# Kernel optimization log

Hardware: AMD Instinct MI355X
Metric: run time of the kernel (lower is better)

The kernel has to match this reference:

```python
import jax, jax.numpy as jnp
import numpy as np

B, S, D_IN = 16, 4096, 1024
H, HD = 8, 64            # num_heads, head_dim
V = H * HD               # value_dim = 512
F_OUT = 120              # forecast_horizon
EPS = 1e-5


def _rotate(x):
    # theta_shift in the source ignores sin/cos: stack((-x2, x1)) and flatten
    x1 = x[..., 0::2]
    x2 = x[..., 1::2]
    return jnp.stack((-x2, x1), axis=-1).reshape(x.shape)


def setup_inputs() -> dict:
    key = jax.random.key(0)
    kx, kq, kk, kv, ko, _ = jax.random.split(key, 6)
    return {
        "x": jax.random.normal(kx, (B, S, D_IN), dtype=jnp.float32),
        "Wq": jax.random.normal(kq, (V, D_IN), dtype=jnp.float32) * 0.02,
        "Wk": jax.random.normal(kk, (V, D_IN), dtype=jnp.float32) * 0.02,
        "Wv": jax.random.normal(kv, (V, D_IN), dtype=jnp.float32) * 0.02,
        "Wout": jax.random.normal(ko, (F_OUT, V), dtype=jnp.float32) * 0.02,
        "gamma": jnp.ones((V,), dtype=jnp.float32),  # RMSNorm weight
    }


def reference(x, Wq, Wk, Wv, Wout, gamma):
    b, s, _ = x.shape
    scaling = HD ** -0.5
    q = (x @ Wq.T) * scaling          # [B,S,V]
    k = (x @ Wk.T) * scaling
    v = (x @ Wv.T).reshape(b, H, s, HD)   # raw view reinterpretation (as in torch)
    qr = _rotate(q).reshape(b, H, s, HD)  # raw view, matches torch .view
    kr = _rotate(k).reshape(b, H, s, HD)
    # recurrent_forward with incremental_state=None:
    # kv = 0.9*0 + 0.1*(kr*v); output = sum_s(qr*kv); scale = S
    kv = 0.1 * (kr * v)
    out = jnp.sum(qr * kv, axis=2) / jnp.float32(s)  # [B,H,HD]
    out = out.reshape(b, H * HD)                      # [B,V]
    # RMSNorm
    rms = out * jax.lax.rsqrt(jnp.mean(out * out, axis=-1, keepdims=True) + EPS) * gamma
    g = jax.nn.gelu(rms, approximate=False)  # torch F.gelu default = exact erf
    return g @ Wout.T                         # [B, forecast_horizon]
```

## Files before the change

kernel.cpp:

```cpp
#include <hip/hip_runtime.h>
#include <hip/hip_bf16.h>
#include <math.h>

#define B_   16
#define S_   4096
#define DIN  1024
#define V_   512
#define FOUT 120

typedef __attribute__((ext_vector_type(8))) short bf16x8;
typedef __attribute__((ext_vector_type(4))) float f32x4;

#define AS1 __attribute__((address_space(1)))
#define AS3 __attribute__((address_space(3)))

__device__ const float CSCALE = 0.1f / (64.0f * 4096.0f);
__device__ const float EPSF = 1e-5f;

__device__ inline void gl2lds16(const void* g, void* l) {
  __builtin_amdgcn_global_load_lds((const AS1 unsigned int*)g,
                                   (AS3 unsigned int*)l, 16, 0, 0);
}

__device__ inline unsigned short f2b(float f) {
  unsigned u = __builtin_bit_cast(unsigned, f);
  unsigned r = (u + 0x7FFFu + ((u >> 16) & 1u)) >> 16;
  return (unsigned short)r;
}

__device__ inline bf16x8 pack8(float4 a, float4 b) {
  bf16x8 r;
  r[0] = (short)f2b(a.x); r[1] = (short)f2b(a.y);
  r[2] = (short)f2b(a.z); r[3] = (short)f2b(a.w);
  r[4] = (short)f2b(b.x); r[5] = (short)f2b(b.y);
  r[6] = (short)f2b(b.z); r[7] = (short)f2b(b.w);
  return r;
}

__global__ void msr_convw(const float* __restrict__ Wq, const float* __restrict__ Wk,
                          const float* __restrict__ Wv, unsigned short* __restrict__ Wt) {
  int e = blockIdx.x * 256 + threadIdx.x;
  int l = e & 63;
  int f = (e >> 6) % 24;
  int ck = (e >> 6) / 24;
  int k = ck & 31;
  int ct = ck >> 5;
  int nf = f / 3, g = f % 3;
  const float* W = (g == 0) ? Wq : (g == 1) ? Wk : Wv;
  int ch = ct * 128 + nf * 16 + (l & 15);
  const float* src = W + (size_t)ch * DIN + k * 32 + (l >> 4) * 8;
  float4 a = *(const float4*)src;
  float4 b = *(const float4*)(src + 4);
  *(bf16x8*)(Wt + (size_t)e * 8) = pack8(a, b);
}

__global__ __launch_bounds__(256) void msr_convx(const float* __restrict__ x,
                                                 unsigned short* __restrict__ Xb) {
  const size_t stride = (size_t)gridDim.x * 256;
  for (size_t i = blockIdx.x * 256ull + threadIdx.x; i < 8388608ull; i += stride) {
    const float* src = x + i * 8;
    float4 a = *(const float4*)src;
    float4 b = *(const float4*)(src + 4);
    *(bf16x8*)(Xb + i * 8) = pack8(a, b);
  }
}

#define WAITVM7  asm volatile("s_waitcnt vmcnt(7)" ::: "memory")
#define WAITVM0  asm volatile("s_waitcnt vmcnt(0)" ::: "memory")
#define WAITLGKM asm volatile("s_waitcnt lgkmcnt(0)" ::: "memory")
#define SCHEDB   __builtin_amdgcn_sched_barrier(0)
#define BARRIER  { asm volatile("" ::: "memory"); __builtin_amdgcn_s_barrier(); asm volatile("" ::: "memory"); }

template <bool DIRECT>
__global__ __launch_bounds__(256, 2) void msr_main(
    const float* __restrict__ x, const unsigned short* __restrict__ Xb,
    const unsigned short* __restrict__ Wt, float* __restrict__ outacc) {
  const int bid = blockIdx.x;
  const int xcd = bid & 7;
  const int j = bid >> 3;
  const int ct = j & 3;
  const int rt = xcd * 128 + (j >> 2);
  const int r0 = rt << 6;

  __shared__ __align__(16) unsigned char smem_[81920];

  const int t = threadIdx.x;
  const int w = t >> 6, lane = t & 63;
  const int w6 = w * 6;
  const int l16 = lane * 16;

  const unsigned short* pWt =
      Wt + (((size_t)ct * 32) * 24 + w6) * 512 + (size_t)lane * 8;
  const unsigned short* pXa = Xb + (size_t)(r0 + (t >> 2)) * DIN + (t & 3) * 8;
  const float* pXf = x + (size_t)(r0 + (t >> 2)) * DIN + (t & 3) * 8;
  const int awoff = (((t >> 2) >> 4) * 64 + (t & 3) * 16 + ((t >> 2) & 15)) * 16;

  f32x4 acc[3][4][2];
#pragma unroll
  for (int g = 0; g < 3; ++g)
#pragma unroll
    for (int m = 0; m < 4; ++m)
#pragma unroll
      for (int n = 0; n < 2; ++n) acc[g][m][n] = (f32x4){0.f, 0.f, 0.f, 0.f};

  bf16x8 afr[4], bfr0[3], bfr1[3];
  bf16x8 xE, xO;

#define ALOAD(REG, PX, PXF, C2) { \
  if constexpr (DIRECT) { \
    const unsigned short* _p = (PX) + (size_t)(C2) * 32; \
    asm volatile("global_load_dwordx4 %0, %1, off" : "=v"(REG) : "v"(_p) : "memory"); \
  } else { \
    const float* _pf = (PXF) + (size_t)(C2) * 32; \
    REG = pack8(*(const float4*)_pf, *(const float4*)(_pf + 4)); \
  } }

#define STAGEB(PW, C2, SB) { \
  _Pragma("unroll") for (int i = 0; i < 6; ++i) \
    gl2lds16((PW) + (size_t)(C2) * 12288 + i * 512, \
             smem_ + 8192 + (SB) * 24576 + (w6 + i) * 1024); }

#define READS(KB, AB) { \
  _Pragma("unroll") for (int m = 0; m < 4; ++m) \
    afr[m] = *(const bf16x8*)(smem_ + (AB) * 4096 + (m * 64 + lane) * 16); \
  _Pragma("unroll") for (int g = 0; g < 3; ++g) \
    bfr0[g] = *(const bf16x8*)(smem_ + 8192 + (KB) * 24576 + (w6 + g) * 1024 + l16); \
  _Pragma("unroll") for (int g = 0; g < 3; ++g) \
    bfr1[g] = *(const bf16x8*)(smem_ + 8192 + (KB) * 24576 + (w6 + 3 + g) * 1024 + l16); }

#define MFMAP { \
  __builtin_amdgcn_s_setprio(1); \
  _Pragma("unroll") for (int g = 0; g < 3; ++g) \
  _Pragma("unroll") for (int m = 0; m < 4; ++m) { \
    acc[g][m][0] = __builtin_amdgcn_mfma_f32_16x16x32_bf16(afr[m], bfr0[g], acc[g][m][0], 0, 0, 0); \
    acc[g][m][1] = __builtin_amdgcn_mfma_f32_16x16x32_bf16(afr[m], bfr1[g], acc[g][m][1], 0, 0, 0); \
  } \
  __builtin_amdgcn_s_setprio(0); }

#define STEP(KB, AB, SB, C2, REGW, REGL) { \
  READS(KB, AB); \
  STAGEB(pWi, C2, SB); \
  ALOAD(REGL, pXi, pXfi, C2); \
  SCHEDB; \
  MFMAP; \
  WAITVM7; \
  *(bf16x8*)(smem_ + ((AB) ^ 1) * 4096 + awoff) = REGW; \
  WAITLGKM; \
  BARRIER; }

  ALOAD(xE, pXa, pXf, 0);
  STAGEB(pWt, 0, 0);
  STAGEB(pWt, 1, 1);
  ALOAD(xO, pXa, pXf, 1);
  if constexpr (DIRECT) { asm volatile("s_waitcnt vmcnt(13)" ::: "memory"); }
  *(bf16x8*)(smem_ + awoff) = xE;
  WAITVM7;
  WAITLGKM;
  BARRIER;

  const unsigned short* pWi = pWt;
  const unsigned short* pXi = pXa;
  const float* pXfi = pXf;
#pragma unroll 1
  for (int i = 0; i < 5; ++i) {
    STEP(0, 0, 2, 2, xO, xE);
    STEP(1, 1, 0, 3, xE, xO);
    STEP(2, 0, 1, 4, xO, xE);
    STEP(0, 1, 2, 5, xE, xO);
    STEP(1, 0, 0, 6, xO, xE);
    STEP(2, 1, 1, 7, xE, xO);
    pWi += 6 * 12288;
    pXi += 6 * 32;
    pXfi += 6 * 32;
  }
  READS(0, 0);
  SCHEDB;
  MFMAP;
  WAITVM0;
  *(bf16x8*)(smem_ + 4096 + awoff) = xO;
  WAITLGKM;
  BARRIER;
  READS(1, 1);
  MFMAP;
#undef STEP
#undef MFMAP
#undef READS
#undef STAGEB
#undef ALOAD

  float pd0 = 0.f, pd1 = 0.f;
#pragma unroll
  for (int m = 0; m < 4; ++m)
#pragma unroll
    for (int r = 0; r < 4; ++r) {
      float qk0 = acc[0][m][0][r] * acc[1][m][0][r];
      float qk1 = acc[0][m][1][r] * acc[1][m][1][r];
      pd0 += __shfl_xor(qk0, 1, 64) * acc[2][m][0][r];
      pd1 += __shfl_xor(qk1, 1, 64) * acc[2][m][1][r];
    }
  pd0 += __shfl_xor(pd0, 16, 64); pd0 += __shfl_xor(pd0, 32, 64);
  pd1 += __shfl_xor(pd1, 16, 64); pd1 += __shfl_xor(pd1, 32, 64);

  if (lane < 16) {
    float* dst = &outacc[((rt >> 3) << 6) + (w & 1) * 32 + lane];
    atomicAdd(dst, pd0);
    atomicAdd(dst + 16, pd1);
  }
}

__global__ __launch_bounds__(256) void msr_finish(
    const float* __restrict__ outacc, const float* __restrict__ gamma,
    const float* __restrict__ Wout, float* __restrict__ y) {
  const int b = blockIdx.x;
  const int t = threadIdx.x;
  __shared__ float g[V_];
  __shared__ float wsum[4];

  float v0 = outacc[b * V_ + t] * CSCALE;
  float v1 = outacc[b * V_ + 256 + t] * CSCALE;
  float ss = v0 * v0 + v1 * v1;
#pragma unroll
  for (int o = 32; o > 0; o >>= 1) ss += __shfl_down(ss, o, 64);
  if ((t & 63) == 0) wsum[t >> 6] = ss;
  __syncthreads();
  float tot = wsum[0] + wsum[1] + wsum[2] + wsum[3];
  float rs = rsqrtf(tot * (1.0f / (float)V_) + EPSF);

  float r0v = v0 * rs * gamma[t];
  float r1v = v1 * rs * gamma[t + 256];
  g[t]       = 0.5f * r0v * (1.0f + erff(r0v * 0.70710678118654752f));
  g[t + 256] = 0.5f * r1v * (1.0f + erff(r1v * 0.70710678118654752f));
  __syncthreads();

  if (t < FOUT) {
    const float* wr = Wout + (size_t)t * V_;
    float acc = 0.f;
#pragma unroll 4
    for (int c = 0; c < V_; c += 4) {
      float4 w4 = *(const float4*)(wr + c);
      acc += g[c] * w4.x + g[c + 1] * w4.y + g[c + 2] * w4.z + g[c + 3] * w4.w;
    }
    y[b * FOUT + t] = acc;
  }
}

extern "C" void kernel_launch(void* const* d_in, const int* in_sizes, int n_in,
                              void* d_out, int out_size, void* d_ws, size_t ws_size,
                              hipStream_t stream) {
  const float* x     = (const float*)d_in[0];
  const float* Wq    = (const float*)d_in[1];
  const float* Wk    = (const float*)d_in[2];
  const float* Wv    = (const float*)d_in[3];
  const float* Wout  = (const float*)d_in[4];
  const float* gamma = (const float*)d_in[5];

  float* outacc = (float*)d_ws;
  unsigned short* Wt = (unsigned short*)((char*)d_ws + 32768);
  unsigned short* Xb = (unsigned short*)((char*)d_ws + 32768 + 3145728);
  float* y = (float*)d_out;

  const size_t need = 32768ull + 3145728ull + 134217728ull;

  msr_convw<<<768, 256, 0, stream>>>(Wq, Wk, Wv, Wt);
  hipMemsetAsync(outacc, 0, B_ * V_ * sizeof(float), stream);

  if (ws_size >= need) {
    msr_convx<<<2048, 256, 0, stream>>>(x, Xb);
    msr_main<true><<<4096, 256, 0, stream>>>(x, Xb, Wt, outacc);
  } else {
    msr_main<false><<<4096, 256, 0, stream>>>(x, Xb, Wt, outacc);
  }
  msr_finish<<<B_, 256, 0, stream>>>(outacc, gamma, Wout, y);
}
```

Baseline: 301.3 us.

## Drop x bf16 pre-conversion pass and load weight fragments directly into registers

Removes the separate x-to-bf16 conversion kernel and its 128 MiB workspace buffer. The main kernel now reads fp32 x directly and packs it to bf16 in registers. Weight B-fragments are loaded straight from global into double-buffered registers instead of being staged through LDS with global_load_lds, which shrinks LDS from 80 KiB to 8 KiB. This avoids an extra full write and read of x, at the cost of twice the global x bytes per block, more register pressure, and no explicit vmcnt pipelining.

```diff
diff --git a/kernel.cpp b/kernel.cpp
--- a/kernel.cpp
+++ b/kernel.cpp
@@ -11,16 +11,8 @@
 typedef __attribute__((ext_vector_type(8))) short bf16x8;
 typedef __attribute__((ext_vector_type(4))) float f32x4;
 
-#define AS1 __attribute__((address_space(1)))
-#define AS3 __attribute__((address_space(3)))
-
 __device__ const float CSCALE = 0.1f / (64.0f * 4096.0f);
 __device__ const float EPSF = 1e-5f;
-
-__device__ inline void gl2lds16(const void* g, void* l) {
-  __builtin_amdgcn_global_load_lds((const AS1 unsigned int*)g,
-                                   (AS3 unsigned int*)l, 16, 0, 0);
-}
 
 __device__ inline unsigned short f2b(float f) {
   unsigned u = __builtin_bit_cast(unsigned, f);
@@ -54,27 +46,12 @@
   *(bf16x8*)(Wt + (size_t)e * 8) = pack8(a, b);
 }
 
-__global__ __launch_bounds__(256) void msr_convx(const float* __restrict__ x,
-                                                 unsigned short* __restrict__ Xb) {
-  const size_t stride = (size_t)gridDim.x * 256;
-  for (size_t i = blockIdx.x * 256ull + threadIdx.x; i < 8388608ull; i += stride) {
-    const float* src = x + i * 8;
-    float4 a = *(const float4*)src;
-    float4 b = *(const float4*)(src + 4);
-    *(bf16x8*)(Xb + i * 8) = pack8(a, b);
-  }
-}
-
-#define WAITVM7  asm volatile("s_waitcnt vmcnt(7)" ::: "memory")
-#define WAITVM0  asm volatile("s_waitcnt vmcnt(0)" ::: "memory")
 #define WAITLGKM asm volatile("s_waitcnt lgkmcnt(0)" ::: "memory")
-#define SCHEDB   __builtin_amdgcn_sched_barrier(0)
 #define BARRIER  { asm volatile("" ::: "memory"); __builtin_amdgcn_s_barrier(); asm volatile("" ::: "memory"); }
 
-template <bool DIRECT>
 __global__ __launch_bounds__(256, 2) void msr_main(
-    const float* __restrict__ x, const unsigned short* __restrict__ Xb,
-    const unsigned short* __restrict__ Wt, float* __restrict__ outacc) {
+    const float* __restrict__ x, const unsigned short* __restrict__ Wt,
+    float* __restrict__ outacc) {
   const int bid = blockIdx.x;
   const int xcd = bid & 7;
   const int j = bid >> 3;
@@ -82,17 +59,16 @@
   const int rt = xcd * 128 + (j >> 2);
   const int r0 = rt << 6;
 
-  __shared__ __align__(16) unsigned char smem_[81920];
+  __shared__ __align__(16) unsigned char smem_[8192];
 
   const int t = threadIdx.x;
   const int w = t >> 6, lane = t & 63;
   const int w6 = w * 6;
-  const int l16 = lane * 16;
-
-  const unsigned short* pWt =
+
+  const unsigned short* pB =
       Wt + (((size_t)ct * 32) * 24 + w6) * 512 + (size_t)lane * 8;
-  const unsigned short* pXa = Xb + (size_t)(r0 + (t >> 2)) * DIN + (t & 3) * 8;
-  const float* pXf = x + (size_t)(r0 + (t >> 2)) * DIN + (t & 3) * 8;
+
+  const float* pX = x + (size_t)(r0 + (t >> 2)) * DIN + (t & 3) * 8;
   const int awoff = (((t >> 2) >> 4) * 64 + (t & 3) * 16 + ((t >> 2) & 15)) * 16;
 
   f32x4 acc[3][4][2];
@@ -103,90 +79,55 @@
 #pragma unroll
       for (int n = 0; n < 2; ++n) acc[g][m][n] = (f32x4){0.f, 0.f, 0.f, 0.f};
 
-  bf16x8 afr[4], bfr0[3], bfr1[3];
-  bf16x8 xE, xO;
-
-#define ALOAD(REG, PX, PXF, C2) { \
-  if constexpr (DIRECT) { \
-    const unsigned short* _p = (PX) + (size_t)(C2) * 32; \
-    asm volatile("global_load_dwordx4 %0, %1, off" : "=v"(REG) : "v"(_p) : "memory"); \
-  } else { \
-    const float* _pf = (PXF) + (size_t)(C2) * 32; \
-    REG = pack8(*(const float4*)_pf, *(const float4*)(_pf + 4)); \
-  } }
-
-#define STAGEB(PW, C2, SB) { \
+  bf16x8 afr[4], bE[6], bO[6];
+  float4 xE0, xE1, xO0, xO1;
+
+#define LOADB(dst, kk) { \
+  const unsigned short* _pb = pB + (size_t)(kk) * 12288; \
   _Pragma("unroll") for (int i = 0; i < 6; ++i) \
-    gl2lds16((PW) + (size_t)(C2) * 12288 + i * 512, \
-             smem_ + 8192 + (SB) * 24576 + (w6 + i) * 1024); }
-
-#define READS(KB, AB) { \
+    dst[i] = *(const bf16x8*)(_pb + i * 512); }
+
+#define READS(AB) { \
   _Pragma("unroll") for (int m = 0; m < 4; ++m) \
-    afr[m] = *(const bf16x8*)(smem_ + (AB) * 4096 + (m * 64 + lane) * 16); \
-  _Pragma("unroll") for (int g = 0; g < 3; ++g) \
-    bfr0[g] = *(const bf16x8*)(smem_ + 8192 + (KB) * 24576 + (w6 + g) * 1024 + l16); \
-  _Pragma("unroll") for (int g = 0; g < 3; ++g) \
-    bfr1[g] = *(const bf16x8*)(smem_ + 8192 + (KB) * 24576 + (w6 + 3 + g) * 1024 + l16); }
-
-#define MFMAP { \
+    afr[m] = *(const bf16x8*)(smem_ + (AB) * 4096 + (m * 64 + lane) * 16); }
+
+#define MFMAP(BF) { \
   __builtin_amdgcn_s_setprio(1); \
   _Pragma("unroll") for (int g = 0; g < 3; ++g) \
   _Pragma("unroll") for (int m = 0; m < 4; ++m) { \
-    acc[g][m][0] = __builtin_amdgcn_mfma_f32_16x16x32_bf16(afr[m], bfr0[g], acc[g][m][0], 0, 0, 0); \
-    acc[g][m][1] = __builtin_amdgcn_mfma_f32_16x16x32_bf16(afr[m], bfr1[g], acc[g][m][1], 0, 0, 0); \
+    acc[g][m][0] = __builtin_amdgcn_mfma_f32_16x16x32_bf16(afr[m], BF[g],     acc[g][m][0], 0, 0, 0); \
+    acc[g][m][1] = __builtin_amdgcn_mfma_f32_16x16x32_bf16(afr[m], BF[3 + g], acc[g][m][1], 0, 0, 0); \
   } \
   __builtin_amdgcn_s_setprio(0); }
 
-#define STEP(KB, AB, SB, C2, REGW, REGL) { \
-  READS(KB, AB); \
-  STAGEB(pWi, C2, SB); \
-  ALOAD(REGL, pXi, pXfi, C2); \
-  SCHEDB; \
-  MFMAP; \
-  WAITVM7; \
-  *(bf16x8*)(smem_ + ((AB) ^ 1) * 4096 + awoff) = REGW; \
+#define STEP(AB, CUR, NXT, KK, WR0, WR1, LD0, LD1) { \
+  READS(AB); \
+  { const int _kb = ((KK) + 1 < 31) ? (KK) + 1 : 31; LOADB(NXT, _kb); } \
+  { const int _kx = ((KK) + 2 < 31) ? (KK) + 2 : 31; \
+    const float* _px = pX + _kx * 32; \
+    LD0 = *(const float4*)_px; LD1 = *(const float4*)(_px + 4); } \
+  MFMAP(CUR); \
+  *(bf16x8*)(smem_ + (((AB) ^ 1) * 4096) + awoff) = pack8(WR0, WR1); \
   WAITLGKM; \
   BARRIER; }
 
-  ALOAD(xE, pXa, pXf, 0);
-  STAGEB(pWt, 0, 0);
-  STAGEB(pWt, 1, 1);
-  ALOAD(xO, pXa, pXf, 1);
-  if constexpr (DIRECT) { asm volatile("s_waitcnt vmcnt(13)" ::: "memory"); }
-  *(bf16x8*)(smem_ + awoff) = xE;
-  WAITVM7;
+  xE0 = *(const float4*)pX; xE1 = *(const float4*)(pX + 4);
+  *(bf16x8*)(smem_ + awoff) = pack8(xE0, xE1);
+  LOADB(bE, 0);
+  { const float* _px = pX + 32; xO0 = *(const float4*)_px; xO1 = *(const float4*)(_px + 4); }
   WAITLGKM;
   BARRIER;
 
-  const unsigned short* pWi = pWt;
-  const unsigned short* pXi = pXa;
-  const float* pXfi = pXf;
 #pragma unroll 1
-  for (int i = 0; i < 5; ++i) {
-    STEP(0, 0, 2, 2, xO, xE);
-    STEP(1, 1, 0, 3, xE, xO);
-    STEP(2, 0, 1, 4, xO, xE);
-    STEP(0, 1, 2, 5, xE, xO);
-    STEP(1, 0, 0, 6, xO, xE);
-    STEP(2, 1, 1, 7, xE, xO);
-    pWi += 6 * 12288;
-    pXi += 6 * 32;
-    pXfi += 6 * 32;
+  for (int i = 0; i < 16; ++i) {
+    const int k = i * 2;
+    STEP(0, bE, bO, k,     xO0, xO1, xE0, xE1);
+    STEP(1, bO, bE, k + 1, xE0, xE1, xO0, xO1);
   }
-  READS(0, 0);
-  SCHEDB;
-  MFMAP;
-  WAITVM0;
-  *(bf16x8*)(smem_ + 4096 + awoff) = xO;
-  WAITLGKM;
-  BARRIER;
-  READS(1, 1);
-  MFMAP;
 #undef STEP
 #undef MFMAP
 #undef READS
-#undef STAGEB
-#undef ALOAD
+#undef LOADB
 
   float pd0 = 0.f, pd1 = 0.f;
 #pragma unroll
@@ -256,19 +197,10 @@
 
   float* outacc = (float*)d_ws;
   unsigned short* Wt = (unsigned short*)((char*)d_ws + 32768);
-  unsigned short* Xb = (unsigned short*)((char*)d_ws + 32768 + 3145728);
   float* y = (float*)d_out;
-
-  const size_t need = 32768ull + 3145728ull + 134217728ull;
 
   msr_convw<<<768, 256, 0, stream>>>(Wq, Wk, Wv, Wt);
   hipMemsetAsync(outacc, 0, B_ * V_ * sizeof(float), stream);
-
-  if (ws_size >= need) {
-    msr_convx<<<2048, 256, 0, stream>>>(x, Xb);
-    msr_main<true><<<4096, 256, 0, stream>>>(x, Xb, Wt, outacc);
-  } else {
-    msr_main<false><<<4096, 256, 0, stream>>>(x, Xb, Wt, outacc);
-  }
+  msr_main<<<4096, 256, 0, stream>>>(x, Wt, outacc);
   msr_finish<<<B_, 256, 0, stream>>>(outacc, gamma, Wout, y);
 }
```

After: 250.1 us. -17.0%, faster.
